# Performance work log

Hardware: AMD Instinct MI355X
Metric: run time of the kernel (lower is better)

Reference implementation:

```python
import jax, jax.numpy as jnp
import numpy as np

D_K = 64  # per-head key dim, used for 1/sqrt(d_k) scaling

def setup_inputs() -> dict:
    key = jax.random.key(0)
    ks = jax.random.split(key, 5)
    B, S, D, H, DK, DV = 4, 2048, 1024, 16, 64, 64
    # xavier_normal-ish scale for [D, DK] weights
    w_std = float(np.sqrt(2.0 / (D + DK)))
    return {
        "x":  jax.random.normal(ks[0], (B, S, D), dtype=jnp.float32),
        "W_Q": jax.random.normal(ks[1], (H, D, DK), dtype=jnp.float32) * w_std,
        "W_K": jax.random.normal(ks[2], (H, D, DK), dtype=jnp.float32) * w_std,
        "W_V": jax.random.normal(ks[3], (H, D, DV), dtype=jnp.float32) * w_std,
        "W_O": jax.random.normal(ks[4], (H * DV, D), dtype=jnp.float32) * float(np.sqrt(1.0 / (H * DV))),
    }

def reference(x, W_Q, W_K, W_V, W_O):
    # x: [B,S,D]; W_Q/W_K/W_V: [H,D,Dk]; W_O: [H*Dv, D]
    q = jnp.einsum("bsd,hdk->bhsk", x, W_Q)
    k = jnp.einsum("bsd,hdk->bhsk", x, W_K)
    v = jnp.einsum("bsd,hdv->bhsv", x, W_V)
    scale = 1.0 / jnp.sqrt(jnp.asarray(D_K, dtype=x.dtype))
    scores = jnp.einsum("bhsk,bhtk->bhst", q, k) * scale  # [B,H,S,S]
    weights = jax.nn.softmax(scores, axis=-1)
    out = jnp.einsum("bhst,bhtv->bhsv", weights, v)       # [B,H,S,Dv]
    B, H, S, DV = out.shape
    # concat heads in order head0..headH-1 along last dim, matching slice writes
    attn_out = jnp.transpose(out, (0, 2, 1, 3)).reshape(B, S, H * DV)
    return attn_out @ W_O
```

## Files before the change

kernel.cpp:

```cpp
#include <hip/hip_runtime.h>
#include <hip/hip_bf16.h>
#include <math.h>

#define BB 4
#define SS 2048
#define DD 1024
#define HH 16
#define DKV 64

typedef __attribute__((ext_vector_type(8))) short bf16x8;
typedef __attribute__((ext_vector_type(4))) float f32x4;
typedef __attribute__((ext_vector_type(2))) __fp16 f16x2;
typedef __attribute__((ext_vector_type(4))) __fp16 f16x4;
typedef __attribute__((ext_vector_type(8))) __fp16 f16x8;
typedef unsigned short u16;
typedef unsigned int u32;
typedef __attribute__((ext_vector_type(2))) unsigned int u32x2;

__device__ inline u16 f2bf(float f) {
  union { float f; u32 u; } v; v.f = f;
  u32 r = v.u + 0x7FFFu + ((v.u >> 16) & 1u);
  return (u16)(r >> 16);
}
__device__ inline u32 pack2bf(float a, float b) {
  return (u32)f2bf(a) | ((u32)f2bf(b) << 16);
}
__device__ inline u32 pack2h(float a, float b) {
  union { f16x2 h; u32 u; } c;
  c.h = __builtin_amdgcn_cvt_pkrtz(a, b);
  return c.u;
}
__device__ inline void gload16(const u16* g, u16* l) {
  __builtin_amdgcn_global_load_lds(
      (const __attribute__((address_space(1))) u32*)g,
      (__attribute__((address_space(3))) u32*)l, 16, 0, 0);
}

__device__ inline void pl32(u32 a, u32 b, u32& x, u32& y) {
#if __has_builtin(__builtin_amdgcn_permlane32_swap)
  u32x2 r = __builtin_amdgcn_permlane32_swap(a, b, false, false);
  x = r.x; y = r.y;
#else
  const bool hi = (threadIdx.x & 32) != 0;
  u32 as = (u32)__shfl_xor((int)a, 32);
  u32 bs = (u32)__shfl_xor((int)b, 32);
  x = hi ? bs : a;
  y = hi ? b : as;
#endif
}
__device__ inline void pl16(u32 a, u32 b, u32& x, u32& y) {
#if __has_builtin(__builtin_amdgcn_permlane16_swap)
  u32x2 r = __builtin_amdgcn_permlane16_swap(a, b, false, false);
  x = r.x; y = r.y;
#else
  const bool odd = (threadIdx.x & 16) != 0;
  u32 as = (u32)__shfl_xor((int)a, 16);
  u32 bs = (u32)__shfl_xor((int)b, 16);
  x = odd ? bs : a;
  y = odd ? b : as;
#endif
}

__global__ __launch_bounds__(256) void cvt_x(const float* __restrict__ x,
                                             u16* __restrict__ xb) {
  const long i = ((long)blockIdx.x * 256 + threadIdx.x) * 4;
  const float4 v = *(const float4*)&x[i];
  uint2 o = {pack2bf(v.x, v.y), pack2bf(v.z, v.w)};
  *(uint2*)&xb[i] = o;
}

__global__ __launch_bounds__(256) void wqkv_trans(
    const float* __restrict__ Wq, const float* __restrict__ Wk,
    const float* __restrict__ Wv, u16* __restrict__ Wt) {
  __shared__ u16 T[64][65];
  const int z = blockIdx.z;
  const int which = z >> 4, h = z & 15;
  const float* inb =
      (which == 0 ? Wq : (which == 1 ? Wk : Wv)) + (long)h * DD * DKV;
  u16* outb = Wt + (long)which * DD * DD + (long)h * DKV * DD;
  const int r0 = blockIdx.x * 64;
  const int t = threadIdx.x;
  const int r = t >> 2, cc = (t & 3) * 16;
#pragma unroll
  for (int j = 0; j < 16; j += 4) {
    const float4 v = *(const float4*)&inb[(long)(r0 + r) * DKV + cc + j];
    T[cc + j + 0][r] = f2bf(v.x);
    T[cc + j + 1][r] = f2bf(v.y);
    T[cc + j + 2][r] = f2bf(v.z);
    T[cc + j + 3][r] = f2bf(v.w);
  }
  __syncthreads();
  const int c = t >> 2, rr = (t & 3) * 16;
  u16 tmp[16];
#pragma unroll
  for (int j = 0; j < 16; ++j) tmp[j] = T[c][rr + j];
  *(uint4*)&outb[(long)c * DD + r0 + rr] = *(uint4*)&tmp[0];
  *(uint4*)&outb[(long)c * DD + r0 + rr + 8] = *(uint4*)&tmp[8];
}

__global__ __launch_bounds__(256) void wo_trans(const float* __restrict__ in,
                                                u16* __restrict__ out) {
  __shared__ u16 T[64][65];
  const int r0 = blockIdx.x * 64, c0 = blockIdx.y * 64;
  const int t = threadIdx.x;
  const int r = t >> 2, cc = (t & 3) * 16;
#pragma unroll
  for (int j = 0; j < 16; j += 4) {
    const float4 v = *(const float4*)&in[(long)(r0 + r) * DD + c0 + cc + j];
    T[cc + j + 0][r] = f2bf(v.x);
    T[cc + j + 1][r] = f2bf(v.y);
    T[cc + j + 2][r] = f2bf(v.z);
    T[cc + j + 3][r] = f2bf(v.w);
  }
  __syncthreads();
  const int c = t >> 2, rr = (t & 3) * 16;
  u16 tmp[16];
#pragma unroll
  for (int j = 0; j < 16; ++j) tmp[j] = T[c][rr + j];
  *(uint4*)&out[(long)(c0 + c) * DD + r0 + rr] = *(uint4*)&tmp[0];
  *(uint4*)&out[(long)(c0 + c) * DD + r0 + rr + 8] = *(uint4*)&tmp[8];
}

__global__ __launch_bounds__(256) void gemm_qkv(
    const u16* __restrict__ xb, const u16* __restrict__ Wt,
    u16* __restrict__ Q, u16* __restrict__ K, u16* __restrict__ Vt) {
  __shared__ u16 Xs[128][32];
  __shared__ u16 Ws[128][32];
  const int tid = threadIdx.x;
  const int wv = tid >> 6, lane = tid & 63;
  const int quad = lane >> 4, ln = lane & 15;
  const int m0 = blockIdx.x * 128, n0 = blockIdx.y * 128;
  const int mbase = (wv & 1) * 64, nbase = (wv >> 1) * 64;
  f32x4 zero = {0.f, 0.f, 0.f, 0.f};
  f32x4 acc[4][4];
#pragma unroll
  for (int a = 0; a < 4; ++a)
#pragma unroll
    for (int b = 0; b < 4; ++b) acc[a][b] = zero;
  const int srow = wv * 32 + (lane >> 2);
  const int ch = (lane & 3) * 8;
  const u16* gx0 = &xb[(long)(m0 + srow) * DD + ch];
  const u16* gx1 = &xb[(long)(m0 + srow + 16) * DD + ch];
  const u16* gw0 = &Wt[(long)(n0 + srow) * DD + ch];
  const u16* gw1 = &Wt[(long)(n0 + srow + 16) * DD + ch];
  u16* lx0 = &Xs[wv * 32][0];
  u16* lx1 = &Xs[wv * 32 + 16][0];
  u16* lw0 = &Ws[wv * 32][0];
  u16* lw1 = &Ws[wv * 32 + 16][0];
  const int which = n0 >> 10;
  if (which < 2) {
    for (int kt = 0; kt < DD; kt += 32) {
      __syncthreads();
      gload16(gx0, lx0);
      gload16(gx1, lx1);
      gload16(gw0, lw0);
      gload16(gw1, lw1);
      gx0 += 32; gx1 += 32; gw0 += 32; gw1 += 32;
      __syncthreads();
      bf16x8 a[4], b[4];
#pragma unroll
      for (int g = 0; g < 4; ++g) {
        a[g] = *(const bf16x8*)&Xs[mbase + g * 16 + ln][quad * 8];
        b[g] = *(const bf16x8*)&Ws[nbase + g * 16 + ln][quad * 8];
      }
#pragma unroll
      for (int mg = 0; mg < 4; ++mg)
#pragma unroll
        for (int ng = 0; ng < 4; ++ng)
          acc[mg][ng] = __builtin_amdgcn_mfma_f32_16x16x32_bf16(
              b[ng], a[mg], acc[mg][ng], 0, 0, 0);
    }
    const float qs = 0.18033688011112042f;
    u16* O = which == 0 ? Q : K;
    const float sc = which == 0 ? qs : 1.0f;
#pragma unroll
    for (int mg = 0; mg < 4; ++mg) {
      const int m = m0 + mbase + mg * 16 + ln;
      const int b_ = m >> 11, s_ = m & (SS - 1);
#pragma unroll
      for (int ng = 0; ng < 4; ++ng) {
        const int rem = (n0 + nbase + ng * 16 + quad * 4) & 1023;
        const int h = rem >> 6, nv = rem & 63;
        const long off = (((long)b_ * HH + h) * SS + s_) * DKV + nv;
        const f32x4 v = acc[mg][ng];
        uint2 o = {pack2bf(v[0] * sc, v[1] * sc), pack2bf(v[2] * sc, v[3] * sc)};
        *(uint2*)&O[off] = o;
      }
    }
  } else {
    for (int kt = 0; kt < DD; kt += 32) {
      __syncthreads();
      gload16(gx0, lx0);
      gload16(gx1, lx1);
      gload16(gw0, lw0);
      gload16(gw1, lw1);
      gx0 += 32; gx1 += 32; gw0 += 32; gw1 += 32;
      __syncthreads();
      bf16x8 a[4], b[4];
#pragma unroll
      for (int g = 0; g < 4; ++g) {
        a[g] = *(const bf16x8*)&Xs[mbase + g * 16 + ln][quad * 8];
        b[g] = *(const bf16x8*)&Ws[nbase + g * 16 + ln][quad * 8];
      }
#pragma unroll
      for (int mg = 0; mg < 4; ++mg)
#pragma unroll
        for (int ng = 0; ng < 4; ++ng)
          acc[mg][ng] = __builtin_amdgcn_mfma_f32_16x16x32_bf16(
              a[mg], b[ng], acc[mg][ng], 0, 0, 0);
    }
#pragma unroll
    for (int mg = 0; mg < 4; ++mg) {
      const int m = m0 + mbase + mg * 16 + quad * 4;
      const int b_ = m >> 11, s_ = m & (SS - 1);
#pragma unroll
      for (int ng = 0; ng < 4; ++ng) {
        const int rem = (n0 + nbase + ng * 16 + ln) & 1023;
        const int h = rem >> 6, nv = rem & 63;
        const f32x4 v = acc[mg][ng];
        uint2 o = {pack2h(v[0], v[1]), pack2h(v[2], v[3])};
        *(uint2*)&Vt[(((long)b_ * HH + h) * DKV + nv) * SS + s_] = o;
      }
    }
  }
}

__global__ __launch_bounds__(256, 2) void attn_mfma(
    const u16* Qg, const u16* __restrict__ Kg, const u16* __restrict__ Vtg,
    u16* Og) {
  __shared__ u16 Ks[64][72];
  __shared__ u16 Vs[64][140];
  const int tid = threadIdx.x;
  const int wv = tid >> 6, lane = tid & 63;
  const int quad = lane >> 4, ln = lane & 15;
  const long base = (long)blockIdx.y * SS * DKV;
  const int s0 = blockIdx.x * 256;
  bf16x8 qf[4][2];
#pragma unroll
  for (int qg = 0; qg < 4; ++qg)
#pragma unroll
    for (int ks = 0; ks < 2; ++ks)
      qf[qg][ks] = *(const bf16x8*)&Qg[base +
          (long)(s0 + wv * 64 + qg * 16 + ln) * DKV + ks * 32 + quad * 8];
  f32x4 zero = {0.f, 0.f, 0.f, 0.f};
  f32x4 minus8 = {-8.f, -8.f, -8.f, -8.f};
  f32x4 of[4][4];
#pragma unroll
  for (int qg = 0; qg < 4; ++qg)
#pragma unroll
    for (int dvg = 0; dvg < 4; ++dvg) of[qg][dvg] = zero;
  float lp[4] = {0.f, 0.f, 0.f, 0.f};
  const int sr = tid >> 2, sc0 = (tid & 3) * 16;
  const u16* gk = &Kg[base + (long)sr * DKV + sc0];
  const u16* gv = &Vtg[base + (long)sr * SS + sc0];
  uint4 kv0 = *(const uint4*)gk;
  uint4 kv1 = *(const uint4*)(gk + 8);
  uint4 vv0 = *(const uint4*)gv;
  uint4 vv1 = *(const uint4*)(gv + 8);
  for (int t0 = 0; t0 < SS; t0 += 64) {
    __syncthreads();
    *(uint4*)&Ks[sr][sc0] = kv0;
    *(uint4*)&Ks[sr][sc0 + 8] = kv1;
    {
      uint2 lo0 = {vv0.x, vv0.y}, hi0 = {vv0.z, vv0.w};
      uint2 lo1 = {vv1.x, vv1.y}, hi1 = {vv1.z, vv1.w};
      *(uint2*)&Vs[sr][sc0] = lo0;
      *(uint2*)&Vs[sr][sc0 + 4] = hi0;
      *(uint2*)&Vs[sr][sc0 + 8] = lo1;
      *(uint2*)&Vs[sr][sc0 + 12] = hi1;
    }
    __syncthreads();
    if (t0 + 64 < SS) {
      gk += 64 * DKV;
      gv += 64;
      kv0 = *(const uint4*)gk;
      kv1 = *(const uint4*)(gk + 8);
      vv0 = *(const uint4*)gv;
      vv1 = *(const uint4*)(gv + 8);
    }
#pragma unroll
    for (int half = 0; half < 2; ++half) {
      f16x4 pe[4], po[4];
#pragma unroll
      for (int sub = 0; sub < 2; ++sub) {
        const int kg = half * 2 + sub;
        bf16x8 kf0 = *(const bf16x8*)&Ks[kg * 16 + ln][quad * 8];
        bf16x8 kf1 = *(const bf16x8*)&Ks[kg * 16 + ln][32 + quad * 8];
#pragma unroll
        for (int qg = 0; qg < 4; ++qg) {
          f32x4 st = minus8;
          st = __builtin_amdgcn_mfma_f32_16x16x32_bf16(kf0, qf[qg][0], st, 0, 0, 0);
          st = __builtin_amdgcn_mfma_f32_16x16x32_bf16(kf1, qf[qg][1], st, 0, 0, 0);
          f32x4 p;
#pragma unroll
          for (int i = 0; i < 4; ++i) p[i] = __builtin_amdgcn_exp2f(st[i]);
          lp[qg] += (p[0] + p[1]) + (p[2] + p[3]);
          const f16x2 lo = __builtin_amdgcn_cvt_pkrtz(p[0], p[1]);
          const f16x2 hi = __builtin_amdgcn_cvt_pkrtz(p[2], p[3]);
          const f16x4 fr = __builtin_shufflevector(lo, hi, 0, 1, 2, 3);
          if (sub == 0) pe[qg] = fr; else po[qg] = fr;
        }
      }
      f16x8 pb2[4];
#pragma unroll
      for (int qg = 0; qg < 4; ++qg) {
        union { f16x4 h; u32 d[2]; } E, O;
        E.h = pe[qg]; O.h = po[qg];
        u32 dw0, dw1, dw2, dw3;
        {
          u32 x, y; pl32(E.d[0], O.d[0], x, y);
          pl16(x, y, dw0, dw2);
        }
        {
          u32 x, y; pl32(E.d[1], O.d[1], x, y);
          pl16(x, y, dw1, dw3);
        }
        union { u32 d[4]; f16x8 h; } R;
        R.d[0] = dw0; R.d[1] = dw1; R.d[2] = dw2; R.d[3] = dw3;
        pb2[qg] = R.h;
      }
#pragma unroll
      for (int dvg = 0; dvg < 4; ++dvg) {
        const f16x4 v0 = *(const f16x4*)&Vs[dvg * 16 + ln][half * 32 + quad * 8];
        const f16x4 v1 = *(const f16x4*)&Vs[dvg * 16 + ln][half * 32 + quad * 8 + 4];
        const f16x8 vf = __builtin_shufflevector(v0, v1, 0, 1, 2, 3, 4, 5, 6, 7);
#pragma unroll
        for (int qg = 0; qg < 4; ++qg)
          of[qg][dvg] = __builtin_amdgcn_mfma_f32_16x16x32_f16(
              vf, pb2[qg], of[qg][dvg], 0, 0, 0);
      }
    }
  }
#pragma unroll
  for (int qg = 0; qg < 4; ++qg) {
    float l = lp[qg];
    l += __shfl_xor(l, 16);
    l += __shfl_xor(l, 32);
    const float inv = 1.f / l;
    const long row = base + (long)(s0 + wv * 64 + qg * 16 + ln) * DKV;
#pragma unroll
    for (int dvg = 0; dvg < 4; ++dvg) {
      const f32x4 v = of[qg][dvg];
      uint2 o = {pack2bf(v[0] * inv, v[1] * inv), pack2bf(v[2] * inv, v[3] * inv)};
      *(uint2*)&Og[row + dvg * 16 + quad * 4] = o;
    }
  }
}

__global__ __launch_bounds__(256) void gemm_out(
    const u16* __restrict__ A, const u16* __restrict__ Wot,
    float* __restrict__ out) {
  __shared__ u16 Xs[128][32];
  __shared__ u16 Ws[128][32];
  const int tid = threadIdx.x;
  const int wv = tid >> 6, lane = tid & 63;
  const int quad = lane >> 4, ln = lane & 15;
  const int m0 = blockIdx.x * 128, n0 = blockIdx.y * 128;
  const int mbase = (wv & 1) * 64, nbase = (wv >> 1) * 64;
  f32x4 zero = {0.f, 0.f, 0.f, 0.f};
  f32x4 acc[4][4];
#pragma unroll
  for (int a = 0; a < 4; ++a)
#pragma unroll
    for (int b = 0; b < 4; ++b) acc[a][b] = zero;
  const int srow = wv * 32 + (lane >> 2);
  const int ch = (lane & 3) * 8;
  const int am0 = m0 + srow, am1 = m0 + srow + 16;
  const long ac0 = ((long)(am0 >> 11) * HH) * SS * DKV + (long)(am0 & (SS - 1)) * DKV;
  const long ac1 = ((long)(am1 >> 11) * HH) * SS * DKV + (long)(am1 & (SS - 1)) * DKV;
  const u16* gw0 = &Wot[(long)(n0 + srow) * DD + ch];
  const u16* gw1 = &Wot[(long)(n0 + srow + 16) * DD + ch];
  u16* lx0 = &Xs[wv * 32][0];
  u16* lx1 = &Xs[wv * 32 + 16][0];
  u16* lw0 = &Ws[wv * 32][0];
  u16* lw1 = &Ws[wv * 32 + 16][0];
  for (int kt = 0; kt < DD; kt += 32) {
    const long hoff = (long)(kt >> 6) * SS * DKV + (kt & 63) + ch;
    __syncthreads();
    gload16(&A[ac0 + hoff], lx0);
    gload16(&A[ac1 + hoff], lx1);
    gload16(gw0, lw0);
    gload16(gw1, lw1);
    gw0 += 32; gw1 += 32;
    __syncthreads();
    bf16x8 a[4], b[4];
#pragma unroll
    for (int g = 0; g < 4; ++g) {
      a[g] = *(const bf16x8*)&Xs[mbase + g * 16 + ln][quad * 8];
      b[g] = *(const bf16x8*)&Ws[nbase + g * 16 + ln][quad * 8];
    }
#pragma unroll
    for (int mg = 0; mg < 4; ++mg)
#pragma unroll
      for (int ng = 0; ng < 4; ++ng)
        acc[mg][ng] = __builtin_amdgcn_mfma_f32_16x16x32_bf16(
            b[ng], a[mg], acc[mg][ng], 0, 0, 0);
  }
#pragma unroll
  for (int mg = 0; mg < 4; ++mg) {
    const long row = (long)(m0 + mbase + mg * 16 + ln) * DD;
#pragma unroll
    for (int ng = 0; ng < 4; ++ng)
      *(f32x4*)&out[row + n0 + nbase + ng * 16 + quad * 4] = acc[mg][ng];
  }
}

extern "C" void kernel_launch(void* const* d_in, const int* in_sizes, int n_in,
                              void* d_out, int out_size, void* d_ws, size_t ws_size,
                              hipStream_t stream) {
  const float* x  = (const float*)d_in[0];
  const float* Wq = (const float*)d_in[1];
  const float* Wk = (const float*)d_in[2];
  const float* Wv = (const float*)d_in[3];
  const float* Wo = (const float*)d_in[4];
  float* out = (float*)d_out;
  u16* xb  = (u16*)d_ws;
  u16* Wt  = xb + (size_t)8192 * 1024;
  u16* Wot = Wt + (size_t)3072 * 1024;
  u16* Q   = Wot + (size_t)1024 * 1024;
  u16* K   = Q + (size_t)BB * HH * SS * DKV;
  u16* Vt  = K + (size_t)BB * HH * SS * DKV;
  const dim3 blk(256);
  cvt_x<<<dim3(8192), blk, 0, stream>>>(x, xb);
  wqkv_trans<<<dim3(16, 1, 48), blk, 0, stream>>>(Wq, Wk, Wv, Wt);
  wo_trans<<<dim3(16, 16), blk, 0, stream>>>(Wo, Wot);
  gemm_qkv<<<dim3(64, 24), blk, 0, stream>>>(xb, Wt, Q, K, Vt);
  attn_mfma<<<dim3(8, 64), blk, 0, stream>>>(Q, K, Vt, Q);
  gemm_out<<<dim3(64, 8), blk, 0, stream>>>(Q, Wot, out);
}
```

Measured before the change: 267.0 us.

## Double-buffer K/V LDS tiles and raise wave priority around MFMA

The attention kernel now ping-pongs between two LDS buffers for K and V tiles, cutting the two barriers per iteration to one, so stores for the next tile never race with reads of the current one. It also wraps the MFMA groups in s_setprio to favour matrix issue across waves. This doubles LDS use per block (about 54KB), which may limit occupancy against the 2-blocks launch bound, and the priority hints may do little.

```diff
diff --git a/kernel.cpp b/kernel.cpp
--- a/kernel.cpp
+++ b/kernel.cpp
@@ -228,8 +228,8 @@
 __global__ __launch_bounds__(256, 2) void attn_mfma(
     const u16* Qg, const u16* __restrict__ Kg, const u16* __restrict__ Vtg,
     u16* Og) {
-  __shared__ u16 Ks[64][72];
-  __shared__ u16 Vs[64][140];
+  __shared__ u16 Ks[2][64][72];
+  __shared__ u16 Vs[2][64][140];
   const int tid = threadIdx.x;
   const int wv = tid >> 6, lane = tid & 63;
   const int quad = lane >> 4, ln = lane & 15;
@@ -257,19 +257,18 @@
   uint4 kv1 = *(const uint4*)(gk + 8);
   uint4 vv0 = *(const uint4*)gv;
   uint4 vv1 = *(const uint4*)(gv + 8);
-  for (int t0 = 0; t0 < SS; t0 += 64) {
-    __syncthreads();
-    *(uint4*)&Ks[sr][sc0] = kv0;
-    *(uint4*)&Ks[sr][sc0 + 8] = kv1;
+  int buf = 0;
+  for (int t0 = 0; t0 < SS; t0 += 64, buf ^= 1) {
+    *(uint4*)&Ks[buf][sr][sc0] = kv0;
+    *(uint4*)&Ks[buf][sr][sc0 + 8] = kv1;
     {
       uint2 lo0 = {vv0.x, vv0.y}, hi0 = {vv0.z, vv0.w};
       uint2 lo1 = {vv1.x, vv1.y}, hi1 = {vv1.z, vv1.w};
-      *(uint2*)&Vs[sr][sc0] = lo0;
-      *(uint2*)&Vs[sr][sc0 + 4] = hi0;
-      *(uint2*)&Vs[sr][sc0 + 8] = lo1;
-      *(uint2*)&Vs[sr][sc0 + 12] = hi1;
-    }
-    __syncthreads();
+      *(uint2*)&Vs[buf][sr][sc0] = lo0;
+      *(uint2*)&Vs[buf][sr][sc0 + 4] = hi0;
+      *(uint2*)&Vs[buf][sr][sc0 + 8] = lo1;
+      *(uint2*)&Vs[buf][sr][sc0 + 12] = hi1;
+    }
     if (t0 + 64 < SS) {
       gk += 64 * DKV;
       gv += 64;
@@ -278,19 +277,22 @@
       vv0 = *(const uint4*)gv;
       vv1 = *(const uint4*)(gv + 8);
     }
+    __syncthreads();
 #pragma unroll
     for (int half = 0; half < 2; ++half) {
       f16x4 pe[4], po[4];
 #pragma unroll
       for (int sub = 0; sub < 2; ++sub) {
         const int kg = half * 2 + sub;
-        bf16x8 kf0 = *(const bf16x8*)&Ks[kg * 16 + ln][quad * 8];
-        bf16x8 kf1 = *(const bf16x8*)&Ks[kg * 16 + ln][32 + quad * 8];
+        bf16x8 kf0 = *(const bf16x8*)&Ks[buf][kg * 16 + ln][quad * 8];
+        bf16x8 kf1 = *(const bf16x8*)&Ks[buf][kg * 16 + ln][32 + quad * 8];
 #pragma unroll
         for (int qg = 0; qg < 4; ++qg) {
           f32x4 st = minus8;
+          __builtin_amdgcn_s_setprio(1);
           st = __builtin_amdgcn_mfma_f32_16x16x32_bf16(kf0, qf[qg][0], st, 0, 0, 0);
           st = __builtin_amdgcn_mfma_f32_16x16x32_bf16(kf1, qf[qg][1], st, 0, 0, 0);
+          __builtin_amdgcn_s_setprio(0);
           f32x4 p;
 #pragma unroll
           for (int i = 0; i < 4; ++i) p[i] = __builtin_amdgcn_exp2f(st[i]);
@@ -321,13 +323,15 @@
       }
 #pragma unroll
       for (int dvg = 0; dvg < 4; ++dvg) {
-        const f16x4 v0 = *(const f16x4*)&Vs[dvg * 16 + ln][half * 32 + quad * 8];
-        const f16x4 v1 = *(const f16x4*)&Vs[dvg * 16 + ln][half * 32 + quad * 8 + 4];
+        const f16x4 v0 = *(const f16x4*)&Vs[buf][dvg * 16 + ln][half * 32 + quad * 8];
+        const f16x4 v1 = *(const f16x4*)&Vs[buf][dvg * 16 + ln][half * 32 + quad * 8 + 4];
         const f16x8 vf = __builtin_shufflevector(v0, v1, 0, 1, 2, 3, 4, 5, 6, 7);
+        __builtin_amdgcn_s_setprio(1);
 #pragma unroll
         for (int qg = 0; qg < 4; ++qg)
           of[qg][dvg] = __builtin_amdgcn_mfma_f32_16x16x32_f16(
               vf, pb2[qg], of[qg][dvg], 0, 0, 0);
+        __builtin_amdgcn_s_setprio(0);
       }
     }
   }
```

Measured after the change: 269.1 us. About the same (+0.8%).
